# Kernel tuning notes

Hardware: AMD Instinct MI355X
Metric: run time of the kernel (lower is better)

Reference implementation:

```python
import jax, jax.numpy as jnp
import numpy as np

# nuScenes-style config: 6 cams, 4 FPN levels of a 256x704 image
SPATIAL = np.array([[64, 176], [32, 88], [16, 44], [8, 22]], dtype=np.int32)  # (H, W) per level
NUM_CAMS = 6
EMBED = 256      # embed dims C
GROUPS = 8       # attention groups, C % GROUPS == 0
BS = 2
ANCHORS = 900    # queries
PTS = 13         # key points per anchor


def setup_inputs() -> dict:
    key = jax.random.key(0)
    k1, k2, k3 = jax.random.split(key, 3)
    hw = SPATIAL.prod(axis=1)                                   # per-level H*W
    starts = np.concatenate([[0], np.cumsum(hw)[:-1]]).astype(np.int32)
    num_value = NUM_CAMS * int(hw.sum())                        # 6 * 14960 = 89760
    value = jax.random.normal(k1, (BS, num_value, EMBED), jnp.float32)
    input_spatial_shapes = jnp.asarray(np.tile(SPATIAL[None], (NUM_CAMS, 1, 1)))   # [cams, lvls, 2]
    input_level_start_index = jnp.asarray(np.tile(starts[None], (NUM_CAMS, 1)))    # [cams, lvls]
    sampling_locations = jax.random.uniform(k2, (BS, ANCHORS, PTS, NUM_CAMS, 2), jnp.float32)
    attention_weights = jax.random.uniform(k3, (BS, ANCHORS, PTS, NUM_CAMS, SPATIAL.shape[0], GROUPS), jnp.float32)
    return {
        "value": value,
        "input_spatial_shapes": input_spatial_shapes,
        "input_level_start_index": input_level_start_index,
        "sampling_locations": sampling_locations,
        "attention_weights": attention_weights,
    }


def _dfa(value, shapes, starts, loc, weights):
    """Multi-scale multi-camera deformable aggregation (Sparse4D kernel math)."""
    bs, num_value, c = value.shape
    num_cams, num_levels = shapes.shape[:2]
    _, A, P = loc.shape[:3]
    groups = weights.shape[-1]
    gdim = c // groups
    per_cam = num_value // num_cams
    value_c = value.reshape(bs, num_cams, per_cam, c)           # cam-major layout
    b_idx = jnp.arange(bs)[:, None, None, None]
    cam_idx = jnp.arange(num_cams)[None, None, None, :]
    loc_w = loc[..., 0]                                          # [bs, A, P, cams]
    loc_h = loc[..., 1]
    out = jnp.zeros((bs, A, groups, gdim), value.dtype)
    for lvl in range(num_levels):                                # static small loop over levels
        H = int(shapes[0, lvl, 0]); W = int(shapes[0, lvl, 1]); s = int(starts[0, lvl])
        featf = value_c[:, :, s:s + H * W, :]                    # [bs, cams, H*W, c]
        h = loc_h * H - 0.5
        w = loc_w * W - 0.5
        h0 = jnp.floor(h); w0 = jnp.floor(w)
        dh = h - h0; dw = w - w0
        h0i = h0.astype(jnp.int32); w0i = w0.astype(jnp.int32)

        def corner(hi, wi, bw):
            valid = (hi >= 0) & (hi < H) & (wi >= 0) & (wi < W)  # zero padding outside
            idx = jnp.clip(hi, 0, H - 1) * W + jnp.clip(wi, 0, W - 1)
            v = featf[b_idx, cam_idx, idx]                       # gather -> [bs, A, P, cams, c]
            return v * (bw * valid)[..., None]

        samp = (corner(h0i,     w0i,     (1 - dh) * (1 - dw))
              + corner(h0i,     w0i + 1, (1 - dh) * dw)
              + corner(h0i + 1, w0i,     dh * (1 - dw))
              + corner(h0i + 1, w0i + 1, dh * dw))               # bilinear sample [bs, A, P, cams, c]
        samp = samp.reshape(bs, A, P, num_cams, groups, gdim)
        out = out + jnp.einsum("bapcgd,bapcg->bagd", samp, weights[..., lvl, :])
    return out.reshape(bs, A, c)


def reference(value, input_spatial_shapes, input_level_start_index, sampling_locations, attention_weights):
    shapes = np.asarray(input_spatial_shapes)
    starts = np.asarray(input_level_start_index)
    return _dfa(value, shapes, starts, sampling_locations, attention_weights)
```

## Files before the change

kernel.cpp:

```cpp
#include <hip/hip_runtime.h>

constexpr int NCAMS   = 6;
constexpr int EMB     = 256;
constexpr int NGROUPS = 8;
constexpr int NLVL    = 4;
constexpr int NPTS    = 13;
constexpr int NPAIR   = NPTS * NCAMS;
constexpr int NWAVES  = 8;

__global__ __launch_bounds__(512)
void dfa_kernel(const float* __restrict__ value,
                const int*   __restrict__ shapes,
                const int*   __restrict__ starts,
                const float* __restrict__ loc,
                const float* __restrict__ attw,
                float*       __restrict__ out,
                int A, int per_cam)
{
    const int tid  = threadIdx.x;
    const int wv   = tid >> 6;
    const int lane = tid & 63;
    const int b = blockIdx.x / A;
    const int a = blockIdx.x - b * A;

    __shared__ int   sH[NLVL], sW[NLVL], sS[NLVL];
    __shared__ float red[NWAVES][EMB];
    if (tid < NLVL) {
        sH[tid] = shapes[tid * 2 + 0];
        sW[tid] = shapes[tid * 2 + 1];
        sS[tid] = starts[tid];
    }
    __syncthreads();

    const int g = lane >> 3;
    const long ba = (long)b * A + a;
    const float* locp = loc  + ba * (NPTS * NCAMS * 2);
    const float* awp  = attw + ba * (NPTS * NCAMS * NLVL * NGROUPS) + g;

    float4 acc = make_float4(0.f, 0.f, 0.f, 0.f);

    for (int pair = wv; pair < NPAIR; pair += NWAVES) {
        const int p = pair / NCAMS;
        const int c = pair - p * NCAMS;
        const float lw = locp[pair * 2 + 0];
        const float lh = locp[pair * 2 + 1];
        const float* vb = value + ((long)(b * NCAMS + c) * per_cam) * EMB + lane * 4;
        const float* awpc = awp + pair * (NLVL * NGROUPS);

        #pragma unroll
        for (int lvl = 0; lvl < NLVL; ++lvl) {
            const int H = sH[lvl], W = sW[lvl], S = sS[lvl];
            const float hf = lh * (float)H - 0.5f;
            const float wf = lw * (float)W - 0.5f;
            const float h0f = floorf(hf), w0f = floorf(wf);
            const float dh = hf - h0f, dw = wf - w0f;
            const int h0 = (int)h0f, w0 = (int)w0f;
            const int h1 = h0 + 1,  w1 = w0 + 1;

            const float aw = awpc[lvl * NGROUPS];

            float w00 = (1.f - dh) * (1.f - dw) * aw;
            float w01 = (1.f - dh) * dw         * aw;
            float w10 = dh         * (1.f - dw) * aw;
            float w11 = dh         * dw         * aw;

            const bool vh0 = (unsigned)h0 < (unsigned)H;
            const bool vh1 = (unsigned)h1 < (unsigned)H;
            const bool vw0 = (unsigned)w0 < (unsigned)W;
            const bool vw1 = (unsigned)w1 < (unsigned)W;
            w00 = (vh0 && vw0) ? w00 : 0.f;
            w01 = (vh0 && vw1) ? w01 : 0.f;
            w10 = (vh1 && vw0) ? w10 : 0.f;
            w11 = (vh1 && vw1) ? w11 : 0.f;

            const int h0c = min(max(h0, 0), H - 1);
            const int h1c = min(max(h1, 0), H - 1);
            const int w0c = min(max(w0, 0), W - 1);
            const int w1c = min(max(w1, 0), W - 1);

            const float* r0 = vb + (long)(S + h0c * W) * EMB;
            const float* r1 = vb + (long)(S + h1c * W) * EMB;

            const float4 v00 = *(const float4*)(r0 + (long)w0c * EMB);
            const float4 v01 = *(const float4*)(r0 + (long)w1c * EMB);
            const float4 v10 = *(const float4*)(r1 + (long)w0c * EMB);
            const float4 v11 = *(const float4*)(r1 + (long)w1c * EMB);

            acc.x += v00.x * w00 + v01.x * w01 + v10.x * w10 + v11.x * w11;
            acc.y += v00.y * w00 + v01.y * w01 + v10.y * w10 + v11.y * w11;
            acc.z += v00.z * w00 + v01.z * w01 + v10.z * w10 + v11.z * w11;
            acc.w += v00.w * w00 + v01.w * w01 + v10.w * w10 + v11.w * w11;
        }
    }

    *(float4*)&red[wv][lane * 4] = acc;
    __syncthreads();

    if (tid < EMB) {
        float o = red[0][tid];
        #pragma unroll
        for (int w = 1; w < NWAVES; ++w) o += red[w][tid];
        out[ba * EMB + tid] = o;
    }
}

extern "C" void kernel_launch(void* const* d_in, const int* in_sizes, int n_in,
                              void* d_out, int out_size, void* d_ws, size_t ws_size,
                              hipStream_t stream) {
    const float* value  = (const float*)d_in[0];
    const int*   shapes = (const int*)d_in[1];
    const int*   starts = (const int*)d_in[2];
    const float* loc    = (const float*)d_in[3];
    const float* attw   = (const float*)d_in[4];
    float*       out    = (float*)d_out;

    const int B = 2;
    const int A = out_size / (EMB * B);
    const int per_cam = in_sizes[0] / (B * EMB * NCAMS);

    dim3 grid(B * A);
    dim3 block(512);
    dfa_kernel<<<grid, block, 0, stream>>>(value, shapes, starts, loc, attw, out,
                                           A, per_cam);
}
```

Before: 460.1 us.

## Double-buffer bilinear corner loads across point-camera pairs in registers

Splits each point-camera pair into an issue step (address math plus the 16 float4 corner loads and weights into registers) and a consume step (FMA accumulation). The loop is software-pipelined with two register buffers, so the loads for the next pair are in flight while the current pair is accumulated, hiding gather latency. The final cross-wave reduction is also split so all 512 threads each sum four partials. This raises register pressure by roughly 160 extra VGPRs per thread, which can lower occupancy.

```diff
diff --git a/kernel.cpp b/kernel.cpp
--- a/kernel.cpp
+++ b/kernel.cpp
@@ -7,6 +7,76 @@
 constexpr int NPTS    = 13;
 constexpr int NPAIR   = NPTS * NCAMS;
 constexpr int NWAVES  = 8;
+
+
+__device__ __forceinline__ void issue_pair(
+    int pair,
+    const float* __restrict__ value,
+    const float* __restrict__ locp,
+    const float* __restrict__ awp_g,
+    int b, int per_cam, int lane,
+    const int H_[NLVL], const int W_[NLVL], const int S_[NLVL],
+    float4 d[16], float wg[16])
+{
+    const int p = pair / NCAMS;
+    const int c = pair - p * NCAMS;
+    const float lw = locp[pair * 2 + 0];
+    const float lh = locp[pair * 2 + 1];
+    const float* vb = value + ((long)(b * NCAMS + c) * per_cam) * EMB + lane * 4;
+    const float* awpc = awp_g + pair * (NLVL * NGROUPS);
+
+    #pragma unroll
+    for (int lvl = 0; lvl < NLVL; ++lvl) {
+        const int H = H_[lvl], W = W_[lvl], S = S_[lvl];
+        const float hf = lh * (float)H - 0.5f;
+        const float wf = lw * (float)W - 0.5f;
+        const float h0f = floorf(hf), w0f = floorf(wf);
+        const float dh = hf - h0f, dw = wf - w0f;
+        const int h0 = (int)h0f, w0 = (int)w0f;
+        const int h1 = h0 + 1,  w1 = w0 + 1;
+
+        const float aw = awpc[lvl * NGROUPS];
+
+        const float w00 = (1.f - dh) * (1.f - dw) * aw;
+        const float w01 = (1.f - dh) * dw         * aw;
+        const float w10 = dh         * (1.f - dw) * aw;
+        const float w11 = dh         * dw         * aw;
+
+        const bool vh0 = (unsigned)h0 < (unsigned)H;
+        const bool vh1 = (unsigned)h1 < (unsigned)H;
+        const bool vw0 = (unsigned)w0 < (unsigned)W;
+        const bool vw1 = (unsigned)w1 < (unsigned)W;
+        wg[lvl * 4 + 0] = (vh0 && vw0) ? w00 : 0.f;
+        wg[lvl * 4 + 1] = (vh0 && vw1) ? w01 : 0.f;
+        wg[lvl * 4 + 2] = (vh1 && vw0) ? w10 : 0.f;
+        wg[lvl * 4 + 3] = (vh1 && vw1) ? w11 : 0.f;
+
+        const int h0c = min(max(h0, 0), H - 1);
+        const int h1c = min(max(h1, 0), H - 1);
+        const int w0c = min(max(w0, 0), W - 1);
+        const int w1c = min(max(w1, 0), W - 1);
+
+        const float* r0 = vb + (long)(S + h0c * W) * EMB;
+        const float* r1 = vb + (long)(S + h1c * W) * EMB;
+
+        d[lvl * 4 + 0] = *(const float4*)(r0 + (long)w0c * EMB);
+        d[lvl * 4 + 1] = *(const float4*)(r0 + (long)w1c * EMB);
+        d[lvl * 4 + 2] = *(const float4*)(r1 + (long)w0c * EMB);
+        d[lvl * 4 + 3] = *(const float4*)(r1 + (long)w1c * EMB);
+    }
+}
+
+__device__ __forceinline__ void consume_pair(const float4 d[16], const float wg[16],
+                                             float4& acc)
+{
+    #pragma unroll
+    for (int k = 0; k < 16; ++k) {
+        acc.x = fmaf(d[k].x, wg[k], acc.x);
+        acc.y = fmaf(d[k].y, wg[k], acc.y);
+        acc.z = fmaf(d[k].z, wg[k], acc.z);
+        acc.w = fmaf(d[k].w, wg[k], acc.w);
+    }
+}
 
 __global__ __launch_bounds__(512)
 void dfa_kernel(const float* __restrict__ value,
@@ -32,75 +102,50 @@
     }
     __syncthreads();
 
+    int H_[NLVL], W_[NLVL], S_[NLVL];
+    #pragma unroll
+    for (int l = 0; l < NLVL; ++l) { H_[l] = sH[l]; W_[l] = sW[l]; S_[l] = sS[l]; }
+
     const int g = lane >> 3;
     const long ba = (long)b * A + a;
     const float* locp = loc  + ba * (NPTS * NCAMS * 2);
     const float* awp  = attw + ba * (NPTS * NCAMS * NLVL * NGROUPS) + g;
 
     float4 acc = make_float4(0.f, 0.f, 0.f, 0.f);
+    float4 dA[16], dB[16];
+    float  wA[16], wB[16];
 
-    for (int pair = wv; pair < NPAIR; pair += NWAVES) {
-        const int p = pair / NCAMS;
-        const int c = pair - p * NCAMS;
-        const float lw = locp[pair * 2 + 0];
-        const float lh = locp[pair * 2 + 1];
-        const float* vb = value + ((long)(b * NCAMS + c) * per_cam) * EMB + lane * 4;
-        const float* awpc = awp + pair * (NLVL * NGROUPS);
-
-        #pragma unroll
-        for (int lvl = 0; lvl < NLVL; ++lvl) {
-            const int H = sH[lvl], W = sW[lvl], S = sS[lvl];
-            const float hf = lh * (float)H - 0.5f;
-            const float wf = lw * (float)W - 0.5f;
-            const float h0f = floorf(hf), w0f = floorf(wf);
-            const float dh = hf - h0f, dw = wf - w0f;
-            const int h0 = (int)h0f, w0 = (int)w0f;
-            const int h1 = h0 + 1,  w1 = w0 + 1;
-
-            const float aw = awpc[lvl * NGROUPS];
-
-            float w00 = (1.f - dh) * (1.f - dw) * aw;
-            float w01 = (1.f - dh) * dw         * aw;
-            float w10 = dh         * (1.f - dw) * aw;
-            float w11 = dh         * dw         * aw;
-
-            const bool vh0 = (unsigned)h0 < (unsigned)H;
-            const bool vh1 = (unsigned)h1 < (unsigned)H;
-            const bool vw0 = (unsigned)w0 < (unsigned)W;
-            const bool vw1 = (unsigned)w1 < (unsigned)W;
-            w00 = (vh0 && vw0) ? w00 : 0.f;
-            w01 = (vh0 && vw1) ? w01 : 0.f;
-            w10 = (vh1 && vw0) ? w10 : 0.f;
-            w11 = (vh1 && vw1) ? w11 : 0.f;
-
-            const int h0c = min(max(h0, 0), H - 1);
-            const int h1c = min(max(h1, 0), H - 1);
-            const int w0c = min(max(w0, 0), W - 1);
-            const int w1c = min(max(w1, 0), W - 1);
-
-            const float* r0 = vb + (long)(S + h0c * W) * EMB;
-            const float* r1 = vb + (long)(S + h1c * W) * EMB;
-
-            const float4 v00 = *(const float4*)(r0 + (long)w0c * EMB);
-            const float4 v01 = *(const float4*)(r0 + (long)w1c * EMB);
-            const float4 v10 = *(const float4*)(r1 + (long)w0c * EMB);
-            const float4 v11 = *(const float4*)(r1 + (long)w1c * EMB);
-
-            acc.x += v00.x * w00 + v01.x * w01 + v10.x * w10 + v11.x * w11;
-            acc.y += v00.y * w00 + v01.y * w01 + v10.y * w10 + v11.y * w11;
-            acc.z += v00.z * w00 + v01.z * w01 + v10.z * w10 + v11.z * w11;
-            acc.w += v00.w * w00 + v01.w * w01 + v10.w * w10 + v11.w * w11;
-        }
+    int j = wv;
+    issue_pair(j, value, locp, awp, b, per_cam, lane, H_, W_, S_, dA, wA);
+    j += NWAVES;
+    while (j + NWAVES < NPAIR) {
+        issue_pair(j, value, locp, awp, b, per_cam, lane, H_, W_, S_, dB, wB);
+        consume_pair(dA, wA, acc);
+        issue_pair(j + NWAVES, value, locp, awp, b, per_cam, lane, H_, W_, S_, dA, wA);
+        consume_pair(dB, wB, acc);
+        j += 2 * NWAVES;
+    }
+    if (j < NPAIR) {
+        issue_pair(j, value, locp, awp, b, per_cam, lane, H_, W_, S_, dB, wB);
+        consume_pair(dA, wA, acc);
+        consume_pair(dB, wB, acc);
+    } else {
+        consume_pair(dA, wA, acc);
     }
 
     *(float4*)&red[wv][lane * 4] = acc;
     __syncthreads();
 
-    if (tid < EMB) {
-        float o = red[0][tid];
-        #pragma unroll
-        for (int w = 1; w < NWAVES; ++w) o += red[w][tid];
-        out[ba * EMB + tid] = o;
+    float s0 = 0.f;
+    if (tid < 256) {
+        s0 = red[0][tid] + red[1][tid] + red[2][tid] + red[3][tid];
+    } else {
+        const int t = tid - 256;
+        red[4][t] = red[4][t] + red[5][t] + red[6][t] + red[7][t];
+    }
+    __syncthreads();
+    if (tid < 256) {
+        out[ba * EMB + tid] = s0 + red[4][tid];
     }
 }
 
```

After: 445.0 us. 3.3% less time.
